# Kernel optimization log

Hardware: AMD Instinct MI355X
Metric: run time of the kernel (lower is better)

## Reference

```python
import jax, jax.numpy as jnp
import numpy as np

ROPE_BASE = 10000.0

def rotate_half(x):
    d = x.shape[-1] // 2
    return jnp.concatenate([-x[..., d:], x[..., :d]], axis=-1)

def rope_cos_sin(seq_len, head_dim, dtype=jnp.float32):
    inv_freq = 1.0 / (ROPE_BASE ** (jnp.arange(0, head_dim, 2, dtype=jnp.float32) / head_dim))
    t = jnp.arange(seq_len, dtype=jnp.float32)
    freqs = jnp.outer(t, inv_freq)              # [T, hd/2]
    emb = jnp.concatenate([freqs, freqs], axis=-1)  # [T, hd]
    return jnp.cos(emb).astype(dtype), jnp.sin(emb).astype(dtype)

def alibi_slopes(num_heads):
    return jnp.asarray([2.0 ** (-8.0 * i / num_heads) for i in range(1, num_heads + 1)], dtype=jnp.float32)

def setup_inputs() -> dict:
    key = jax.random.key(0)
    k1, k2, k3 = jax.random.split(key, 3)
    B, T, H = 2, 2048, 1024
    return {
        "q": jax.random.normal(k1, (B, T, H), dtype=jnp.float32),
        "k": jax.random.normal(k2, (B, T, H), dtype=jnp.float32),
        "v": jax.random.normal(k3, (B, T, H), dtype=jnp.float32),
        "num_heads": 16,
    }

def reference(q, k, v, num_heads):
    B, T, H = q.shape
    nh = num_heads
    hd = H // nh
    q = q.reshape(B, T, nh, hd)
    k = k.reshape(B, T, nh, hd)
    v = v.reshape(B, T, nh, hd)
    cos, sin = rope_cos_sin(T, hd, q.dtype)      # [T, hd]
    cos = cos[None, :, None, :]                  # [1, T, 1, hd]
    sin = sin[None, :, None, :]
    q = q * cos + rotate_half(q) * sin
    k = k * cos + rotate_half(k) * sin
    # ALiBi additive bias: [nh, T, T]
    rel = jnp.arange(T)[None, :] - jnp.arange(T)[:, None]   # memory - context
    bias = alibi_slopes(nh)[:, None, None] * rel.astype(q.dtype)
    scale = 1.0 / jnp.sqrt(jnp.asarray(hd, dtype=q.dtype))
    scores = jnp.einsum('bqhd,bkhd->bhqk', q, k) * scale + bias[None]
    attn = jax.nn.softmax(scores, axis=-1)
    out = jnp.einsum('bhqk,bkhd->bqhd', attn, v)
    return out.reshape(B, T, H)
```

## Files before the change

kernel.cpp:

```cpp
#include <hip/hip_runtime.h>
#include <math.h>

#define TB 2
#define TT 2048
#define NH 16
#define HD 64
#define HSZ 1024
#define NROW 65536
#define OPHALF 4194304

typedef float floatx4 __attribute__((ext_vector_type(4)));
typedef __bf16 bf16x4 __attribute__((ext_vector_type(4)));
typedef __bf16 bf16x8 __attribute__((ext_vector_type(8)));

#define LOG2E  1.4426950408889634f
#define NEGF   (-0.4152410118609203f)
#define INV2PI 0.15915494309189535f

__global__ __launch_bounds__(256)
void prep_kernel(const float* __restrict__ K, const float* __restrict__ V,
                 __bf16* __restrict__ Kp, __bf16* __restrict__ Vp) {
    int blk = blockIdx.x;
    int kt = blk & 31;
    int bh = blk >> 5;
    int b = bh >> 4, h = bh & 15;
    int tid = threadIdx.x;

    {
        int key = tid >> 2, qq = tid & 3;
        int tglob = kt * 64 + key;
        const float* krow = K + ((size_t)(b * TT + tglob)) * HSZ + h * HD + qq * 8;
        float x0[8], x1[8];
        *(floatx4*)&x0[0] = *(const floatx4*)&krow[0];
        *(floatx4*)&x0[4] = *(const floatx4*)&krow[4];
        *(floatx4*)&x1[0] = *(const floatx4*)&krow[32];
        *(floatx4*)&x1[4] = *(const floatx4*)&krow[36];
        bf16x8 y0, y1;
        #pragma unroll
        for (int j = 0; j < 8; ++j) {
            float freq = exp2f((float)(qq * 8 + j) * NEGF);
            float rv = (float)tglob * freq * INV2PI;
            rv -= floorf(rv);
            float s = __builtin_amdgcn_sinf(rv);
            float c = __builtin_amdgcn_cosf(rv);
            y0[j] = (__bf16)(x0[j] * c - x1[j] * s);
            y1[j] = (__bf16)(x1[j] * c + x0[j] * s);
        }
        size_t base = ((size_t)blk * 4 + (key & 3)) * 1024 + (size_t)(qq * 16 + (key >> 2)) * 8;
        *(bf16x8*)(Kp + base)       = y0;
        *(bf16x8*)(Kp + base + 512) = y1;
    }

    __shared__ __bf16 lt[64][72];
    {
        int vkey = tid >> 2, dg = (tid & 3) * 16;
        const float* vrow = V + ((size_t)(b * TT + kt * 64 + vkey)) * HSZ + h * HD + dg;
        floatx4 v0 = *(const floatx4*)&vrow[0];
        floatx4 v1 = *(const floatx4*)&vrow[4];
        floatx4 v2 = *(const floatx4*)&vrow[8];
        floatx4 v3 = *(const floatx4*)&vrow[12];
        #pragma unroll
        for (int j = 0; j < 4; ++j) {
            lt[dg + j][vkey]      = (__bf16)v0[j];
            lt[dg + 4 + j][vkey]  = (__bf16)v1[j];
            lt[dg + 8 + j][vkey]  = (__bf16)v2[j];
            lt[dg + 12 + j][vkey] = (__bf16)v3[j];
        }
    }
    __syncthreads();
    #pragma unroll
    for (int ss = 0; ss < 2; ++ss) {
        int sidx = tid + ss * 256;
        int hg = sidx >> 6;
        int l = sidx & 63;
        int g = hg >> 2, dn = hg & 3;
        int lq = l >> 4, lr = l & 15;
        bf16x8 o = *(const bf16x8*)&lt[dn * 16 + lr][lq * 16 + g * 8];
        *(bf16x8*)(Vp + (size_t)blk * 4096 + (size_t)hg * 512 + (size_t)l * 8) = o;
    }
}

__global__ __launch_bounds__(256, 2)
void attn_kernel(const float* __restrict__ Q, const __bf16* __restrict__ Kp,
                 const __bf16* __restrict__ Vp, __bf16* __restrict__ Op,
                 float* __restrict__ lp) {
    int blk0 = blockIdx.x;
    int blk = (blk0 & 7) * 128 + (blk0 >> 3);

    int s = blk & 1;
    int qb = (blk >> 1) & 15;
    int bh = blk >> 5;
    int b = bh >> 4, h = bh & 15;
    int tid = threadIdx.x;
    int wave = tid >> 6, lane = tid & 63;
    int lane15 = lane & 15, quad = lane >> 4;

    const float scale2 = 0.125f * LOG2E;
    const float slope2 = exp2f(-0.5f * (float)(h + 1)) * LOG2E;
    const float ms     = slope2 * 2047.0f + 20.0f;

    int qbase = qb * 128 + wave * 32;
    int d0 = quad * 8;
    bf16x8 aQ0[2], aQ1[2];
    #pragma unroll
    for (int qf = 0; qf < 2; ++qf) {
        int t_q = qbase + qf * 16 + lane15;
        const float* qrow = Q + ((size_t)(b * TT + t_q) * HSZ) + h * HD;
        float q0[8], q1[8];
        *(floatx4*)&q0[0] = *(const floatx4*)&qrow[d0];
        *(floatx4*)&q0[4] = *(const floatx4*)&qrow[d0 + 4];
        *(floatx4*)&q1[0] = *(const floatx4*)&qrow[d0 + 32];
        *(floatx4*)&q1[4] = *(const floatx4*)&qrow[d0 + 36];
        #pragma unroll
        for (int j = 0; j < 8; ++j) {
            float freq = exp2f((float)(d0 + j) * NEGF);
            float rv = (float)t_q * freq * INV2PI;
            rv -= floorf(rv);
            float sn = __builtin_amdgcn_sinf(rv);
            float cs = __builtin_amdgcn_cosf(rv);
            aQ0[qf][j] = (__bf16)((q0[j] * cs - q1[j] * sn) * scale2);
            aQ1[qf][j] = (__bf16)((q1[j] * cs + q0[j] * sn) * scale2);
        }
    }

    const float qb16  = slope2 * (float)(16 * quad) - ms;
    const float dstep = slope2 * 64.0f;

    floatx4 O[2][4];
    float lrow[2];
    #pragma unroll
    for (int qf = 0; qf < 2; ++qf) {
        lrow[qf] = 0.f;
        #pragma unroll
        for (int r = 0; r < 4; ++r)
            O[qf][r] = (floatx4){0.f, 0.f, 0.f, 0.f};
    }

    const __bf16* Kb = Kp + (size_t)bh * (TT * HD) + (size_t)lane * 8;
    const __bf16* Vb = Vp + (size_t)bh * (TT * HD) + (size_t)lane * 8;

    const int kt0 = s * 16, kt1 = s * 16 + 16;

    bf16x8 bk[4][2];
    {
        const __bf16* kbase = Kb + (size_t)kt0 * 4096;
        #pragma unroll
        for (int nt = 0; nt < 4; ++nt) {
            bk[nt][0] = *(const bf16x8*)(kbase + nt * 1024);
            bk[nt][1] = *(const bf16x8*)(kbase + nt * 1024 + 512);
        }
    }

    #pragma unroll 1
    for (int kt = kt0; kt < kt1; ++kt) {
        const __bf16* vbase = Vb + (size_t)kt * 4096;
        bf16x8 bv[2][4];
        #pragma unroll
        for (int hg = 0; hg < 8; ++hg)
            bv[hg >> 2][hg & 3] = *(const bf16x8*)(vbase + hg * 512);

        float biasq = qb16 + dstep * (float)kt;

        {
            floatx4 acc[4];
            #pragma unroll
            for (int nt = 0; nt < 4; ++nt) {
                floatx4 a = {0.f, 0.f, 0.f, 0.f};
                a = __builtin_amdgcn_mfma_f32_16x16x32_bf16(bk[nt][0], aQ0[0], a, 0, 0, 0);
                a = __builtin_amdgcn_mfma_f32_16x16x32_bf16(bk[nt][1], aQ1[0], a, 0, 0, 0);
                acc[nt] = a;
            }
            #pragma unroll
            for (int g = 0; g < 2; ++g) {
                bf16x8 aP;
                float ps = 0.f;
                #pragma unroll
                for (int j = 0; j < 8; ++j) {
                    int nt = j & 3, r = g * 2 + (j >> 2);
                    float p = __builtin_amdgcn_exp2f(
                        acc[nt][r] + fmaf(slope2, (float)(4 * r + nt), biasq));
                    ps += p;
                    aP[j] = (__bf16)p;
                }
                lrow[0] += ps;
                O[0][0] = __builtin_amdgcn_mfma_f32_16x16x32_bf16(aP, bv[g][0], O[0][0], 0, 0, 0);
                O[0][1] = __builtin_amdgcn_mfma_f32_16x16x32_bf16(aP, bv[g][1], O[0][1], 0, 0, 0);
                O[0][2] = __builtin_amdgcn_mfma_f32_16x16x32_bf16(aP, bv[g][2], O[0][2], 0, 0, 0);
                O[0][3] = __builtin_amdgcn_mfma_f32_16x16x32_bf16(aP, bv[g][3], O[0][3], 0, 0, 0);
            }
        }

        {
            floatx4 acc[4];
            #pragma unroll
            for (int nt = 0; nt < 4; ++nt) {
                floatx4 a = {0.f, 0.f, 0.f, 0.f};
                a = __builtin_amdgcn_mfma_f32_16x16x32_bf16(bk[nt][0], aQ0[1], a, 0, 0, 0);
                a = __builtin_amdgcn_mfma_f32_16x16x32_bf16(bk[nt][1], aQ1[1], a, 0, 0, 0);
                acc[nt] = a;
            }

            if (kt + 1 < kt1) {
                const __bf16* kbase = Kb + (size_t)(kt + 1) * 4096;
                #pragma unroll
                for (int nt = 0; nt < 4; ++nt) {
                    bk[nt][0] = *(const bf16x8*)(kbase + nt * 1024);
                    bk[nt][1] = *(const bf16x8*)(kbase + nt * 1024 + 512);
                }
            }

            #pragma unroll
            for (int g = 0; g < 2; ++g) {
                bf16x8 aP;
                float ps = 0.f;
                #pragma unroll
                for (int j = 0; j < 8; ++j) {
                    int nt = j & 3, r = g * 2 + (j >> 2);
                    float p = __builtin_amdgcn_exp2f(
                        acc[nt][r] + fmaf(slope2, (float)(4 * r + nt), biasq));
                    ps += p;
                    aP[j] = (__bf16)p;
                }
                lrow[1] += ps;
                O[1][0] = __builtin_amdgcn_mfma_f32_16x16x32_bf16(aP, bv[g][0], O[1][0], 0, 0, 0);
                O[1][1] = __builtin_amdgcn_mfma_f32_16x16x32_bf16(aP, bv[g][1], O[1][1], 0, 0, 0);
                O[1][2] = __builtin_amdgcn_mfma_f32_16x16x32_bf16(aP, bv[g][2], O[1][2], 0, 0, 0);
                O[1][3] = __builtin_amdgcn_mfma_f32_16x16x32_bf16(aP, bv[g][3], O[1][3], 0, 0, 0);
            }
        }
    }

    #pragma unroll
    for (int qf = 0; qf < 2; ++qf) {
        float l = lrow[qf];
        l += __shfl_xor(l, 16);
        l += __shfl_xor(l, 32);
        int q0 = qbase + qf * 16;
        if (quad == 0) {
            int ridl = (b * TT + q0 + lane15) * NH + h;
            lp[s * NROW + ridl] = l;
        }
        #pragma unroll
        for (int r = 0; r < 4; ++r) {
            int rid = (b * TT + q0 + quad * 4 + r) * NH + h;
            size_t base = ((size_t)s * NROW + rid) * HD + lane15;
            Op[base +  0] = (__bf16)O[qf][0][r];
            Op[base + 16] = (__bf16)O[qf][1][r];
            Op[base + 32] = (__bf16)O[qf][2][r];
            Op[base + 48] = (__bf16)O[qf][3][r];
        }
    }
}

__global__ __launch_bounds__(256)
void reduce_kernel(const __bf16* __restrict__ Op, const float* __restrict__ lp,
                   float* __restrict__ Out) {
    int i = blockIdx.x * 256 + threadIdx.x;
    size_t f = (size_t)i * 4;
    int rid = (int)(f >> 6);
    bf16x4 a = *(const bf16x4*)(Op + f);
    bf16x4 c = *(const bf16x4*)(Op + OPHALF + f);
    float inv = 1.0f / (lp[rid] + lp[NROW + rid]);
    floatx4 o;
    #pragma unroll
    for (int j = 0; j < 4; ++j)
        o[j] = ((float)a[j] + (float)c[j]) * inv;
    *(floatx4*)(Out + f) = o;
}

extern "C" void kernel_launch(void* const* d_in, const int* in_sizes, int n_in,
                              void* d_out, int out_size, void* d_ws, size_t ws_size,
                              hipStream_t stream) {
    const float* q = (const float*)d_in[0];
    const float* k = (const float*)d_in[1];
    const float* v = (const float*)d_in[2];
    float* out = (float*)d_out;

    char* ws = (char*)d_ws;
    __bf16* Kp = (__bf16*)ws;
    __bf16* Vp = (__bf16*)(ws + (size_t)8 * 1024 * 1024);
    __bf16* Op = (__bf16*)(ws + (size_t)16 * 1024 * 1024);
    float*  lp = (float*)(ws + (size_t)33 * 1024 * 1024);

    prep_kernel<<<dim3(TB * NH * (TT / 64)), 256, 0, stream>>>(k, v, Kp, Vp);
    attn_kernel<<<dim3(TB * NH * 32), 256, 0, stream>>>(q, Kp, Vp, Op, lp);
    reduce_kernel<<<dim3((TB * TT * HSZ / 4) / 256), 256, 0, stream>>>(Op, lp, out);
}
```

Baseline: 144.0 us.

## Double-buffer V tiles and pin scheduling with sched_barrier and setprio

The key loop is unrolled by two, with ping-pong V register buffers, so the next tile's V loads are issued a full iteration ahead instead of at the start of the same iteration. sched_barrier calls pin where the loads sit relative to compute, and s_setprio raises wave priority around the MFMA groups. The row-sum reduction becomes a tree to shorten the dependency chain. The extra live V buffer raises register pressure, and wrapping the prefetch index back to kt0 adds redundant loads on the last iteration.

```diff
diff --git a/kernel.cpp b/kernel.cpp
--- a/kernel.cpp
+++ b/kernel.cpp
@@ -142,91 +142,88 @@
     const int kt0 = s * 16, kt1 = s * 16 + 16;
 
     bf16x8 bk[4][2];
-    {
-        const __bf16* kbase = Kb + (size_t)kt0 * 4096;
+    bf16x8 bvA[2][4], bvB[2][4];
+
+    auto qk = [&](floatx4 (&acc)[4], bf16x8& aq0, bf16x8& aq1) {
+        __builtin_amdgcn_s_setprio(1);
         #pragma unroll
         for (int nt = 0; nt < 4; ++nt) {
-            bk[nt][0] = *(const bf16x8*)(kbase + nt * 1024);
-            bk[nt][1] = *(const bf16x8*)(kbase + nt * 1024 + 512);
-        }
-    }
+            floatx4 a = {0.f, 0.f, 0.f, 0.f};
+            a = __builtin_amdgcn_mfma_f32_16x16x32_bf16(bk[nt][0], aq0, a, 0, 0, 0);
+            a = __builtin_amdgcn_mfma_f32_16x16x32_bf16(bk[nt][1], aq1, a, 0, 0, 0);
+            acc[nt] = a;
+        }
+        __builtin_amdgcn_s_setprio(0);
+    };
+
+    auto softmax_pv = [&](floatx4 (&acc)[4], bf16x8 (&bvt)[2][4],
+                          float& lq, floatx4 (&Oq)[4], float biasq) {
+        #pragma unroll
+        for (int g = 0; g < 2; ++g) {
+            float p[8];
+            #pragma unroll
+            for (int j = 0; j < 8; ++j) {
+                int nt = j & 3, r = g * 2 + (j >> 2);
+                p[j] = __builtin_amdgcn_exp2f(
+                    acc[nt][r] + fmaf(slope2, (float)(4 * r + nt), biasq));
+            }
+            lq += ((p[0] + p[1]) + (p[2] + p[3])) + ((p[4] + p[5]) + (p[6] + p[7]));
+            bf16x8 aP;
+            #pragma unroll
+            for (int j = 0; j < 8; ++j) aP[j] = (__bf16)p[j];
+            __builtin_amdgcn_s_setprio(1);
+            Oq[0] = __builtin_amdgcn_mfma_f32_16x16x32_bf16(aP, bvt[g][0], Oq[0], 0, 0, 0);
+            Oq[1] = __builtin_amdgcn_mfma_f32_16x16x32_bf16(aP, bvt[g][1], Oq[1], 0, 0, 0);
+            Oq[2] = __builtin_amdgcn_mfma_f32_16x16x32_bf16(aP, bvt[g][2], Oq[2], 0, 0, 0);
+            Oq[3] = __builtin_amdgcn_mfma_f32_16x16x32_bf16(aP, bvt[g][3], Oq[3], 0, 0, 0);
+            __builtin_amdgcn_s_setprio(0);
+        }
+    };
+
+    auto load_bv = [&](bf16x8 (&bvt)[2][4], int kt_) {
+        const __bf16* vb = Vb + (size_t)kt_ * 4096;
+        #pragma unroll
+        for (int hg = 0; hg < 8; ++hg)
+            bvt[hg >> 2][hg & 3] = *(const bf16x8*)(vb + hg * 512);
+    };
+    auto load_bk = [&](int kt_) {
+        const __bf16* kb = Kb + (size_t)kt_ * 4096;
+        #pragma unroll
+        for (int nt = 0; nt < 4; ++nt) {
+            bk[nt][0] = *(const bf16x8*)(kb + nt * 1024);
+            bk[nt][1] = *(const bf16x8*)(kb + nt * 1024 + 512);
+        }
+    };
+
+    load_bk(kt0);
+    load_bv(bvA, kt0);
 
     #pragma unroll 1
-    for (int kt = kt0; kt < kt1; ++kt) {
-        const __bf16* vbase = Vb + (size_t)kt * 4096;
-        bf16x8 bv[2][4];
-        #pragma unroll
-        for (int hg = 0; hg < 8; ++hg)
-            bv[hg >> 2][hg & 3] = *(const bf16x8*)(vbase + hg * 512);
-
-        float biasq = qb16 + dstep * (float)kt;
-
+    for (int kt = kt0; kt < kt1; kt += 2) {
         {
+            load_bv(bvB, kt + 1);
+            __builtin_amdgcn_sched_barrier(0);
+            float biasq = qb16 + dstep * (float)kt;
             floatx4 acc[4];
-            #pragma unroll
-            for (int nt = 0; nt < 4; ++nt) {
-                floatx4 a = {0.f, 0.f, 0.f, 0.f};
-                a = __builtin_amdgcn_mfma_f32_16x16x32_bf16(bk[nt][0], aQ0[0], a, 0, 0, 0);
-                a = __builtin_amdgcn_mfma_f32_16x16x32_bf16(bk[nt][1], aQ1[0], a, 0, 0, 0);
-                acc[nt] = a;
-            }
-            #pragma unroll
-            for (int g = 0; g < 2; ++g) {
-                bf16x8 aP;
-                float ps = 0.f;
-                #pragma unroll
-                for (int j = 0; j < 8; ++j) {
-                    int nt = j & 3, r = g * 2 + (j >> 2);
-                    float p = __builtin_amdgcn_exp2f(
-                        acc[nt][r] + fmaf(slope2, (float)(4 * r + nt), biasq));
-                    ps += p;
-                    aP[j] = (__bf16)p;
-                }
-                lrow[0] += ps;
-                O[0][0] = __builtin_amdgcn_mfma_f32_16x16x32_bf16(aP, bv[g][0], O[0][0], 0, 0, 0);
-                O[0][1] = __builtin_amdgcn_mfma_f32_16x16x32_bf16(aP, bv[g][1], O[0][1], 0, 0, 0);
-                O[0][2] = __builtin_amdgcn_mfma_f32_16x16x32_bf16(aP, bv[g][2], O[0][2], 0, 0, 0);
-                O[0][3] = __builtin_amdgcn_mfma_f32_16x16x32_bf16(aP, bv[g][3], O[0][3], 0, 0, 0);
-            }
-        }
-
+            qk(acc, aQ0[0], aQ1[0]);
+            softmax_pv(acc, bvA, lrow[0], O[0], biasq);
+            qk(acc, aQ0[1], aQ1[1]);
+            load_bk(kt + 1);
+            __builtin_amdgcn_sched_barrier(0);
+            softmax_pv(acc, bvA, lrow[1], O[1], biasq);
+        }
         {
+            int kt2 = kt + 2; if (kt2 >= kt1) kt2 = kt0;
+            load_bv(bvA, kt2);
+            __builtin_amdgcn_sched_barrier(0);
+            float biasq = qb16 + dstep * (float)(kt + 1);
             floatx4 acc[4];
-            #pragma unroll
-            for (int nt = 0; nt < 4; ++nt) {
-                floatx4 a = {0.f, 0.f, 0.f, 0.f};
-                a = __builtin_amdgcn_mfma_f32_16x16x32_bf16(bk[nt][0], aQ0[1], a, 0, 0, 0);
-                a = __builtin_amdgcn_mfma_f32_16x16x32_bf16(bk[nt][1], aQ1[1], a, 0, 0, 0);
-                acc[nt] = a;
-            }
-
-            if (kt + 1 < kt1) {
-                const __bf16* kbase = Kb + (size_t)(kt + 1) * 4096;
-                #pragma unroll
-                for (int nt = 0; nt < 4; ++nt) {
-                    bk[nt][0] = *(const bf16x8*)(kbase + nt * 1024);
-                    bk[nt][1] = *(const bf16x8*)(kbase + nt * 1024 + 512);
-                }
-            }
-
-            #pragma unroll
-            for (int g = 0; g < 2; ++g) {
-                bf16x8 aP;
-                float ps = 0.f;
-                #pragma unroll
-                for (int j = 0; j < 8; ++j) {
-                    int nt = j & 3, r = g * 2 + (j >> 2);
-                    float p = __builtin_amdgcn_exp2f(
-                        acc[nt][r] + fmaf(slope2, (float)(4 * r + nt), biasq));
-                    ps += p;
-                    aP[j] = (__bf16)p;
-                }
-                lrow[1] += ps;
-                O[1][0] = __builtin_amdgcn_mfma_f32_16x16x32_bf16(aP, bv[g][0], O[1][0], 0, 0, 0);
-                O[1][1] = __builtin_amdgcn_mfma_f32_16x16x32_bf16(aP, bv[g][1], O[1][1], 0, 0, 0);
-                O[1][2] = __builtin_amdgcn_mfma_f32_16x16x32_bf16(aP, bv[g][2], O[1][2], 0, 0, 0);
-                O[1][3] = __builtin_amdgcn_mfma_f32_16x16x32_bf16(aP, bv[g][3], O[1][3], 0, 0, 0);
-            }
+            qk(acc, aQ0[0], aQ1[0]);
+            softmax_pv(acc, bvB, lrow[0], O[0], biasq);
+            qk(acc, aQ0[1], aQ1[1]);
+            load_bk(kt2);
+            __builtin_amdgcn_sched_barrier(0);
+            softmax_pv(acc, bvB, lrow[1], O[1], biasq);
         }
     }
 
```

Result: slower. 174.6 us (+21.2%).
